# Performance work log

Hardware: AMD Instinct MI355X
Metric: run time of the kernel (lower is better)

Reference implementation:

```python
import jax, jax.numpy as jnp
import numpy as np


def log_g(x):
    # log of g(x) = x + 0.5 if x >= 0 else sigmoid(x)  (minGRU paper Appendix B)
    return jnp.where(x >= 0, jnp.log(jax.nn.relu(x) + 0.5), -jax.nn.softplus(-x))


def parallel_scan_log(log_coeffs, log_values):
    # log_coeffs: [B, T, H]; log_values: [B, T+1, H]
    a_star = jnp.pad(jnp.cumsum(log_coeffs, axis=1), ((0, 0), (1, 0), (0, 0)))  # [B, T+1, H]
    log_h = a_star + jax.lax.cumlogsumexp(log_values - a_star, axis=1)
    return jnp.exp(log_h)  # [B, T+1, H]


def setup_inputs() -> dict:
    key = jax.random.key(0)
    ks = jax.random.split(key, 6)
    B, T, D, H = 4, 4096, 1024, 1024
    scale = 1.0 / np.sqrt(D)
    return {
        "x": jax.random.normal(ks[0], (B, T, D), dtype=jnp.float32),
        "h_0": jax.random.uniform(ks[1], (B, H), dtype=jnp.float32),
        "Wz": jax.random.normal(ks[2], (H, D), dtype=jnp.float32) * scale,
        "bz": jnp.zeros((H,), dtype=jnp.float32),
        "Wh": jax.random.normal(ks[3], (H, D), dtype=jnp.float32) * scale,
        "bh": jnp.zeros((H,), dtype=jnp.float32),
    }


def reference(x, h_0, Wz, bz, Wh, bh):
    T = x.shape[1]
    k = jnp.einsum("btd,hd->bth", x, Wz) + bz          # linear_z(x)
    log_z = -jax.nn.softplus(-k)                          # log sigmoid(k)
    log_coeffs = -jax.nn.softplus(k)                      # log (1 - sigmoid(k))
    log_h_0 = log_g(h_0)[:, None, :]                      # [B, 1, H]
    log_tilde_h = log_g(jnp.einsum("btd,hd->bth", x, Wh) + bh)
    log_values = jnp.concatenate([log_h_0, log_z + log_tilde_h], axis=1)  # [B, T+1, H]
    h = parallel_scan_log(log_coeffs, log_values)
    return h[:, -T:, :]
```

## Files before the change

kernel.cpp:

```cpp
#include <hip/hip_runtime.h>
#include <hip/hip_bf16.h>
#include <hip/hip_fp16.h>

#define B_ 4
#define T_ 4096
#define D_ 1024
#define H_ 1024
#define M_ (B_ * T_)

typedef __attribute__((ext_vector_type(8))) short short8;
typedef __attribute__((ext_vector_type(4))) float f32x4;

__device__ __forceinline__ unsigned short f2bf(float f) {
    unsigned int u = __float_as_uint(f);
    u += 0x7fffu + ((u >> 16) & 1u);
    return (unsigned short)(u >> 16);
}

__global__ __launch_bounds__(256) void convert_all(
    const float* __restrict__ x, const float* __restrict__ wz, const float* __restrict__ wh,
    unsigned short* __restrict__ xb, unsigned short* __restrict__ wzb, unsigned short* __restrict__ whb)
{
    int i = blockIdx.x * 256 + threadIdx.x;
    const float* s; unsigned short* d; int off;
    if (i < 4194304)      { s = x;  d = xb;  off = i; }
    else if (i < 4456448) { s = wz; d = wzb; off = i - 4194304; }
    else                  { s = wh; d = whb; off = i - 4456448; }
    float4 f = ((const float4*)s)[off];
    ushort4 u;
    u.x = f2bf(f.x); u.y = f2bf(f.y); u.z = f2bf(f.z); u.w = f2bf(f.w);
    ((ushort4*)d)[off] = u;
}

__device__ __forceinline__ void async16(const void* g, void* l) {
    __builtin_amdgcn_global_load_lds(
        (__attribute__((address_space(1))) void*)g,
        (__attribute__((address_space(3))) void*)l,
        16, 0, 0);
}

__global__ __launch_bounds__(256) void dual_gemm_kernel(
    const unsigned short* __restrict__ xb,
    const unsigned short* __restrict__ wzb,
    const unsigned short* __restrict__ whb,
    const float* __restrict__ bz,
    const float* __restrict__ bh,
    __half2* __restrict__ av16,
    float2* __restrict__ chunkAV)
{
    __shared__ short8 ldsA[16 * 64];
    __shared__ short8 ldsBz[8 * 64];
    __shared__ short8 ldsBh[8 * 64];

    const int tid   = threadIdx.x;
    const int lane  = tid & 63;
    const int w     = tid >> 6;
    const int whalf = w >> 1;
    const int nhalf = w & 1;
    const int nb    = blockIdx.x >> 7;
    const int mb    = blockIdx.x & 127;
    const int r16   = lane & 15;
    const int q     = lane >> 4;

    const unsigned short* gA[4];
    short8* lA[4];
#pragma unroll
    for (int i = 0; i < 4; ++i) {
        const int j  = 4 * w + i;
        const int rg = j >> 1, kh = j & 1;
        gA[i] = xb + (size_t)(mb * 128 + rg * 16 + r16) * D_ + kh * 32 + q * 8;
        lA[i] = &ldsA[j * 64];
    }
    const unsigned short* gBz[2]; const unsigned short* gBh[2];
    short8 *lBz[2], *lBh[2];
#pragma unroll
    for (int i = 0; i < 2; ++i) {
        const int j  = 2 * w + i;
        const int rg = j >> 1, kh = j & 1;
        gBz[i] = wzb + (size_t)(nb * 64 + rg * 16 + r16) * D_ + kh * 32 + q * 8;
        gBh[i] = whb + (size_t)(nb * 64 + rg * 16 + r16) * D_ + kh * 32 + q * 8;
        lBz[i] = &ldsBz[j * 64];
        lBh[i] = &ldsBh[j * 64];
    }

    f32x4 accz[4][2] = {};
    f32x4 acch[4][2] = {};

    for (int kk = 0; kk < D_; kk += 64) {
        __syncthreads();
#pragma unroll
        for (int i = 0; i < 4; ++i) async16(gA[i] + kk, lA[i]);
#pragma unroll
        for (int i = 0; i < 2; ++i) { async16(gBz[i] + kk, lBz[i]); async16(gBh[i] + kk, lBh[i]); }
        __syncthreads();

#pragma unroll
        for (int kh = 0; kh < 2; ++kh) {
            short8 fa[4], fz[2], fh[2];
#pragma unroll
            for (int gm = 0; gm < 4; ++gm)
                fa[gm] = ldsA[((whalf * 4 + gm) * 2 + kh) * 64 + lane];
#pragma unroll
            for (int gn = 0; gn < 2; ++gn) {
                fz[gn] = ldsBz[((nhalf * 2 + gn) * 2 + kh) * 64 + lane];
                fh[gn] = ldsBh[((nhalf * 2 + gn) * 2 + kh) * 64 + lane];
            }
#pragma unroll
            for (int gm = 0; gm < 4; ++gm)
#pragma unroll
                for (int gn = 0; gn < 2; ++gn) {
                    accz[gm][gn] = __builtin_amdgcn_mfma_f32_16x16x32_bf16(fa[gm], fz[gn], accz[gm][gn], 0, 0, 0);
                    acch[gm][gn] = __builtin_amdgcn_mfma_f32_16x16x32_bf16(fa[gm], fh[gn], acch[gm][gn], 0, 0, 0);
                }
        }
    }

    const int cglob = mb * 2 + whalf;
    const int cc = cglob & 63;
    const int bb = cglob >> 6;
#pragma unroll
    for (int gn = 0; gn < 2; ++gn) {
        const int ncol = nb * 64 + nhalf * 32 + gn * 16 + r16;
        const float bzv = bz[ncol];
        const float bhv = bh[ncol];
        float CA = 1.0f, CV = 0.0f;
#pragma unroll
        for (int gm = 0; gm < 4; ++gm) {
            float LA = 1.0f, LV = 0.0f;
#pragma unroll
            for (int rr = 0; rr < 4; ++rr) {
                float kv = accz[gm][gn][rr] + bzv;
                float hv = acch[gm][gn][rr] + bhv;
                float tk = __expf(-fabsf(kv));
                float ik = 1.0f / (1.0f + tk);
                float sig = (kv >= 0.0f) ? ik : tk * ik;
                float ac  = (kv >= 0.0f) ? tk * ik : ik;
                float th = __expf(-fabsf(hv));
                float ih = 1.0f / (1.0f + th);
                float gh = (hv >= 0.0f) ? (hv + 0.5f) : th * ih;
                float vv = sig * gh;
                const size_t m = (size_t)mb * 128 + whalf * 64 + gm * 16 + q * 4 + rr;
                av16[(size_t)m * H_ + ncol] = __floats2half2_rn(ac, vv);
                LV = ac * LV + vv;
                LA = ac * LA;
            }
#pragma unroll
            for (int mask = 16; mask <= 32; mask <<= 1) {
                float PA = __shfl_xor(LA, mask);
                float PV = __shfl_xor(LV, mask);
                if (lane & mask) { LV = LA * PV + LV; LA = LA * PA; }
                else             { LV = PA * LV + PV; LA = PA * LA; }
            }
            CV = LA * CV + LV;
            CA = LA * CA;
        }
        if (q == 0)
            chunkAV[cc * 4096 + bb * 1024 + ncol] = make_float2(CA, CV);
    }
}

__global__ __launch_bounds__(256) void scan_pass2(const float2* __restrict__ chunkAV,
                                                  const float* __restrict__ h0,
                                                  float* __restrict__ hstart) {
    int chan = blockIdx.x * blockDim.x + threadIdx.x;
    int n = chan & (H_ - 1);
    int b = chan >> 10;
    float x = h0[b * H_ + n];
    float h;
    if (x >= 0.0f) { h = x + 0.5f; }
    else { float t = __expf(x); h = t / (1.0f + t); }
#pragma unroll 8
    for (int c = 0; c < 64; ++c) {
        hstart[c * 4096 + chan] = h;
        float2 s = chunkAV[c * 4096 + chan];
        h = s.x * h + s.y;
    }
}

__global__ __launch_bounds__(256) void scan_pass3(const __half2* __restrict__ av16,
                                                  const float* __restrict__ hstart,
                                                  float* __restrict__ out) {
    int g = blockIdx.x * blockDim.x + threadIdx.x;
    int n = g & (H_ - 1);
    int rest = g >> 10;
    int c = rest & 63;
    int b = rest >> 6;
    float h = hstart[c * 4096 + b * 1024 + n];
    const __half2* base = av16 + ((size_t)(b * T_ + c * 64)) * H_ + n;
    float* obase = out + ((size_t)(b * T_ + c * 64)) * H_ + n;
#pragma unroll 8
    for (int t = 0; t < 64; ++t) {
        float2 p = __half22float2(base[(size_t)t * H_]);
        h = p.x * h + p.y;
        obase[(size_t)t * H_] = h;
    }
}

extern "C" void kernel_launch(void* const* d_in, const int* in_sizes, int n_in,
                              void* d_out, int out_size, void* d_ws, size_t ws_size,
                              hipStream_t stream) {
    const float* x  = (const float*)d_in[0];
    const float* h0 = (const float*)d_in[1];
    const float* Wz = (const float*)d_in[2];
    const float* bz = (const float*)d_in[3];
    const float* Wh = (const float*)d_in[4];
    const float* bh = (const float*)d_in[5];
    float* out = (float*)d_out;

    char* ws = (char*)d_ws;
    unsigned short* xb  = (unsigned short*)(ws);
    unsigned short* wzb = (unsigned short*)(ws + 33554432);
    unsigned short* whb = (unsigned short*)(ws + 35651584);
    __half2* av16       = (__half2*)(ws + 37748736);
    float2* chunkAV     = (float2*)(ws + 104857600);
    float*  hstart      = (float*)(ws + 106954752);

    convert_all<<<18432, 256, 0, stream>>>(x, Wz, Wh, xb, wzb, whb);

    dual_gemm_kernel<<<2048, 256, 0, stream>>>(xb, wzb, whb, bz, bh, av16, chunkAV);

    scan_pass2<<<16,   256, 0, stream>>>(chunkAV, h0, hstart);
    scan_pass3<<<1024, 256, 0, stream>>>(av16, hstart, out);
}
```

Before: 295.9 us.

## Load GEMM fragments directly from global into registers with double buffering

Drops the LDS staging (async global-to-LDS copies plus two barriers per k-step) in the dual GEMM. Each wave now loads its MFMA fragments straight from global memory into registers, with a two-stage register double buffer so the next k-slice loads while the current MFMAs issue. Launch bounds ask for three blocks per SM. This removes barrier and LDS traffic but gives up sharing tiles across waves, so each wave re-reads its A and B rows and leans on L2. The final prefetch also reads one slice past the end of each row.

Measured after the change: 393.9 us. 33.1% more time.

```diff
diff --git a/kernel.cpp b/kernel.cpp
--- a/kernel.cpp
+++ b/kernel.cpp
@@ -32,14 +32,7 @@
     ((ushort4*)d)[off] = u;
 }
 
-__device__ __forceinline__ void async16(const void* g, void* l) {
-    __builtin_amdgcn_global_load_lds(
-        (__attribute__((address_space(1))) void*)g,
-        (__attribute__((address_space(3))) void*)l,
-        16, 0, 0);
-}
-
-__global__ __launch_bounds__(256) void dual_gemm_kernel(
+__global__ __launch_bounds__(256, 3) void dual_gemm_kernel(
     const unsigned short* __restrict__ xb,
     const unsigned short* __restrict__ wzb,
     const unsigned short* __restrict__ whb,
@@ -48,10 +41,6 @@
     __half2* __restrict__ av16,
     float2* __restrict__ chunkAV)
 {
-    __shared__ short8 ldsA[16 * 64];
-    __shared__ short8 ldsBz[8 * 64];
-    __shared__ short8 ldsBh[8 * 64];
-
     const int tid   = threadIdx.x;
     const int lane  = tid & 63;
     const int w     = tid >> 6;
@@ -63,57 +52,48 @@
     const int q     = lane >> 4;
 
     const unsigned short* gA[4];
-    short8* lA[4];
-#pragma unroll
-    for (int i = 0; i < 4; ++i) {
-        const int j  = 4 * w + i;
-        const int rg = j >> 1, kh = j & 1;
-        gA[i] = xb + (size_t)(mb * 128 + rg * 16 + r16) * D_ + kh * 32 + q * 8;
-        lA[i] = &ldsA[j * 64];
-    }
-    const unsigned short* gBz[2]; const unsigned short* gBh[2];
-    short8 *lBz[2], *lBh[2];
-#pragma unroll
-    for (int i = 0; i < 2; ++i) {
-        const int j  = 2 * w + i;
-        const int rg = j >> 1, kh = j & 1;
-        gBz[i] = wzb + (size_t)(nb * 64 + rg * 16 + r16) * D_ + kh * 32 + q * 8;
-        gBh[i] = whb + (size_t)(nb * 64 + rg * 16 + r16) * D_ + kh * 32 + q * 8;
-        lBz[i] = &ldsBz[j * 64];
-        lBh[i] = &ldsBh[j * 64];
+    const unsigned short* gBz[2];
+    const unsigned short* gBh[2];
+#pragma unroll
+    for (int gm = 0; gm < 4; ++gm)
+        gA[gm] = xb + (size_t)(mb * 128 + whalf * 64 + gm * 16 + r16) * D_ + q * 8;
+#pragma unroll
+    for (int gn = 0; gn < 2; ++gn) {
+        gBz[gn] = wzb + (size_t)(nb * 64 + nhalf * 32 + gn * 16 + r16) * D_ + q * 8;
+        gBh[gn] = whb + (size_t)(nb * 64 + nhalf * 32 + gn * 16 + r16) * D_ + q * 8;
     }
 
     f32x4 accz[4][2] = {};
     f32x4 acch[4][2] = {};
 
+    short8 fa0[4], fz0[2], fh0[2];
+    short8 fa1[4], fz1[2], fh1[2];
+
+#define LOADF(fa, fz, fh, off) do {                                              \
+    _Pragma("unroll") for (int i_ = 0; i_ < 4; ++i_)                             \
+        fa[i_] = *(const short8*)(gA[i_] + (off));                               \
+    _Pragma("unroll") for (int i_ = 0; i_ < 2; ++i_) {                           \
+        fz[i_] = *(const short8*)(gBz[i_] + (off));                              \
+        fh[i_] = *(const short8*)(gBh[i_] + (off));                              \
+    } } while (0)
+
+#define MFMAS(fa, fz, fh) do {                                                   \
+    _Pragma("unroll") for (int gm_ = 0; gm_ < 4; ++gm_)                          \
+    _Pragma("unroll") for (int gn_ = 0; gn_ < 2; ++gn_) {                        \
+        accz[gm_][gn_] = __builtin_amdgcn_mfma_f32_16x16x32_bf16(fa[gm_], fz[gn_], accz[gm_][gn_], 0, 0, 0); \
+        acch[gm_][gn_] = __builtin_amdgcn_mfma_f32_16x16x32_bf16(fa[gm_], fh[gn_], acch[gm_][gn_], 0, 0, 0); \
+    } } while (0)
+
+    LOADF(fa0, fz0, fh0, 0);
+#pragma unroll 4
     for (int kk = 0; kk < D_; kk += 64) {
-        __syncthreads();
-#pragma unroll
-        for (int i = 0; i < 4; ++i) async16(gA[i] + kk, lA[i]);
-#pragma unroll
-        for (int i = 0; i < 2; ++i) { async16(gBz[i] + kk, lBz[i]); async16(gBh[i] + kk, lBh[i]); }
-        __syncthreads();
-
-#pragma unroll
-        for (int kh = 0; kh < 2; ++kh) {
-            short8 fa[4], fz[2], fh[2];
-#pragma unroll
-            for (int gm = 0; gm < 4; ++gm)
-                fa[gm] = ldsA[((whalf * 4 + gm) * 2 + kh) * 64 + lane];
-#pragma unroll
-            for (int gn = 0; gn < 2; ++gn) {
-                fz[gn] = ldsBz[((nhalf * 2 + gn) * 2 + kh) * 64 + lane];
-                fh[gn] = ldsBh[((nhalf * 2 + gn) * 2 + kh) * 64 + lane];
-            }
-#pragma unroll
-            for (int gm = 0; gm < 4; ++gm)
-#pragma unroll
-                for (int gn = 0; gn < 2; ++gn) {
-                    accz[gm][gn] = __builtin_amdgcn_mfma_f32_16x16x32_bf16(fa[gm], fz[gn], accz[gm][gn], 0, 0, 0);
-                    acch[gm][gn] = __builtin_amdgcn_mfma_f32_16x16x32_bf16(fa[gm], fh[gn], acch[gm][gn], 0, 0, 0);
-                }
-        }
-    }
+        LOADF(fa1, fz1, fh1, kk + 32);
+        MFMAS(fa0, fz0, fh0);
+        LOADF(fa0, fz0, fh0, kk + 64);
+        MFMAS(fa1, fz1, fh1);
+    }
+#undef LOADF
+#undef MFMAS
 
     const int cglob = mb * 2 + whalf;
     const int cc = cglob & 63;
```
